# Kernel optimization log

Measured on AMD Instinct MI355X. Metric: run time of the kernel, lower is better.

The kernel has to match this reference:

```python
import jax, jax.numpy as jnp
import numpy as np

IN_DIM = 256
INNER = IN_DIM // 8  # 32


def setup_inputs() -> dict:
    key = jax.random.key(0)
    ks = jax.random.split(key, 9)
    B, C, W, H = 4, IN_DIM, 64, 64
    sc = 0.05
    return {
        "x": jax.random.normal(ks[0], (B, C, W, H), dtype=jnp.float32),
        "Wf": jax.random.normal(ks[1], (INNER, C), dtype=jnp.float32) * sc,
        "bf": jnp.zeros((INNER,), dtype=jnp.float32),
        "Wg": jax.random.normal(ks[2], (INNER, C), dtype=jnp.float32) * sc,
        "bg": jnp.zeros((INNER,), dtype=jnp.float32),
        "Wh": jax.random.normal(ks[3], (INNER, C), dtype=jnp.float32) * sc,
        "bh": jnp.zeros((INNER,), dtype=jnp.float32),
        "Wv": jax.random.normal(ks[4], (C, INNER), dtype=jnp.float32) * sc,
        "bv": jnp.zeros((C,), dtype=jnp.float32),
        "gamma": jnp.ones((1,), dtype=jnp.float32) * 0.5,  # nonzero so attention path matters
    }


def reference(x, Wf, bf, Wg, bg, Wh, bh, Wv, bv, gamma):
    B, C, W, H = x.shape
    N = W * H
    xf = x.reshape(B, C, N)
    # 1x1 convs == per-pixel linear projections
    f = jnp.einsum('kc,bcn->bkn', Wf, xf) + bf[None, :, None]  # [B, C/8, N]
    g = jnp.einsum('kc,bcn->bkn', Wg, xf) + bg[None, :, None]
    h = jnp.einsum('kc,bcn->bkn', Wh, xf) + bh[None, :, None]
    # s[b,n,m] = sum_k f[b,k,n] * g[b,k,m]  (f^T @ g)
    s = jnp.einsum('bkn,bkm->bnm', f, g)                      # [B, N, N]
    attn = jax.nn.softmax(s, axis=-1)                          # softmax over last dim
    attn_map = jnp.transpose(attn, (0, 2, 1))                  # returned map (permuted)
    # o_pre = h_x @ attn_map : o_pre[b,k,m] = sum_n h[b,k,n] * attn[b,m,n]
    o_pre = jnp.einsum('bkn,bmn->bkm', h, attn)                # [B, C/8, N]
    o = jnp.einsum('ck,bkn->bcn', Wv, o_pre) + bv[None, :, None]
    o = o.reshape(B, C, W, H)
    y = gamma.reshape(()) * o + x
    return (y, attn_map)
```

## Files before the change

### kernel.cpp

```cpp
#include <hip/hip_runtime.h>
#include <cstddef>
#include <cstdint>

#define NB     4
#define CDIM   256
#define KD     32
#define NPIX   4096
#define SSHIFT 20.0f

typedef __attribute__((ext_vector_type(8))) short  bfrag;
typedef __attribute__((ext_vector_type(4))) float  facc;

#define MFMA(a,b,c) __builtin_amdgcn_mfma_f32_16x16x32_bf16((a),(b),(c),0,0,0)

__device__ __forceinline__ unsigned short f2bf(float x) {
    union { float f; unsigned u; } v; v.f = x;
    unsigned u = v.u + 0x7fffu + ((v.u >> 16) & 1u);
    return (unsigned short)(u >> 16);
}
__device__ __forceinline__ float bf2f(unsigned short h) {
    union { float f; unsigned u; } v; v.u = ((unsigned)h) << 16;
    return v.f;
}

#define OFF_FA_HI (0)
#define OFF_FA_LO (1u<<20)
#define OFF_GB_HI (2u<<20)
#define OFF_GB_LO (3u<<20)
#define OFF_HB    (4u<<20)
#define OFF_WA_HI (5u<<20)
#define OFF_WA_LO ((5u<<20) + 65536)
#define OFF_OT    ((5u<<20) + 131072)

__global__ __launch_bounds__(256) void wt_kernel(const float* __restrict__ Wf,
                                                 const float* __restrict__ Wg,
                                                 const float* __restrict__ Wh,
                                                 unsigned short* __restrict__ WA_hi,
                                                 unsigned short* __restrict__ WA_lo)
{
    int t = blockIdx.x * 256 + threadIdx.x;
    if (t >= 48 * 64) return;
    int tile = t >> 6, lane = t & 63;
    int rt = tile >> 3, cc = tile & 7;
    int q = lane >> 4, c15 = lane & 15;
    int row = rt * 16 + c15;
    const float* W = (row < 32) ? (Wf + (size_t)row * CDIM)
                   : (row < 64) ? (Wg + (size_t)(row - 32) * CDIM)
                                : (Wh + (size_t)(row - 64) * CDIM);
    int cb = cc * 32 + q * 8;
    bfrag vh, vl;
#pragma unroll
    for (int j = 0; j < 8; ++j) {
        float xv = W[cb + j];
        unsigned short h = f2bf(xv);
        vh[j] = (short)h;
        vl[j] = (short)f2bf(xv - bf2f(h));
    }
    *(bfrag*)(WA_hi + (size_t)t * 8) = vh;
    *(bfrag*)(WA_lo + (size_t)t * 8) = vl;
}

__global__ __launch_bounds__(256) void proj_kernel(const float* __restrict__ x,
                                                   const unsigned short* __restrict__ WA_hi,
                                                   const unsigned short* __restrict__ WA_lo,
                                                   const float* __restrict__ bfv,
                                                   const float* __restrict__ bgv,
                                                   const float* __restrict__ bhv,
                                                   unsigned short* __restrict__ fA_hi,
                                                   unsigned short* __restrict__ fA_lo,
                                                   unsigned short* __restrict__ gB_hi,
                                                   unsigned short* __restrict__ gB_lo,
                                                   unsigned short* __restrict__ hB)
{
    __shared__ float xs[32][65];
    __shared__ float os[96][65];
    __shared__ float bias_s[96];

    const int b  = blockIdx.y;
    const int n0 = blockIdx.x * 64;
    const int tid = threadIdx.x;
    const int w = tid >> 6, lane = tid & 63, q = lane >> 4, c15 = lane & 15;

    if (tid < 96)
        bias_s[tid] = (tid < 32) ? bfv[tid] : (tid < 64 ? bgv[tid - 32] : bhv[tid - 64]);

    facc acc[6];
#pragma unroll
    for (int rt = 0; rt < 6; ++rt) acc[rt] = (facc){0.f, 0.f, 0.f, 0.f};

    const float* xb = x + (size_t)b * CDIM * NPIX + n0;
    const int cr = tid >> 3, nb = (tid & 7) * 8;

    for (int cc = 0; cc < 8; ++cc) {
        const float* src = xb + (size_t)(cc * 32 + cr) * NPIX + nb;
        float4 va = *(const float4*)src;
        float4 vb = *(const float4*)(src + 4);
        __syncthreads();
        *(float4*)&xs[cr][nb]     = va;
        *(float4*)&xs[cr][nb + 4] = vb;
        __syncthreads();

        bfrag xh, xl;
#pragma unroll
        for (int j = 0; j < 8; ++j) {
            float xv = xs[q * 8 + j][w * 16 + c15];
            unsigned short h = f2bf(xv);
            xh[j] = (short)h;
            xl[j] = (short)f2bf(xv - bf2f(h));
        }
#pragma unroll
        for (int rt = 0; rt < 6; ++rt) {
            size_t wo = ((size_t)(rt * 8 + cc) * 64 + lane) * 8;
            bfrag wh = *(const bfrag*)(WA_hi + wo);
            bfrag wl = *(const bfrag*)(WA_lo + wo);
            acc[rt] = MFMA(wh, xh, acc[rt]);
            acc[rt] = MFMA(wh, xl, acc[rt]);
            acc[rt] = MFMA(wl, xh, acc[rt]);
        }
    }

#pragma unroll
    for (int rt = 0; rt < 6; ++rt)
#pragma unroll
        for (int i = 0; i < 4; ++i) {
            int row = rt * 16 + q * 4 + i;
            os[row][w * 16 + c15] = acc[rt][i] + bias_s[row];
        }
    __syncthreads();

    {
        bfrag vh, vl;
#pragma unroll
        for (int j = 0; j < 8; ++j) {
            float v = os[q * 8 + j][w * 16 + c15];
            unsigned short h = f2bf(v);
            vh[j] = (short)h; vl[j] = (short)f2bf(v - bf2f(h));
        }
        size_t o = ((size_t)(b * 256 + (n0 >> 4) + w) * 64 + lane) * 8;
        *(bfrag*)(fA_hi + o) = vh;
        *(bfrag*)(fA_lo + o) = vl;
#pragma unroll
        for (int j = 0; j < 8; ++j) {
            float v = os[32 + q * 8 + j][w * 16 + c15];
            unsigned short h = f2bf(v);
            vh[j] = (short)h; vl[j] = (short)f2bf(v - bf2f(h));
        }
        *(bfrag*)(gB_hi + o) = vh;
        *(bfrag*)(gB_lo + o) = vl;
        int mcl = w >> 1, kt = w & 1;
        bfrag hv;
#pragma unroll
        for (int j = 0; j < 8; ++j) {
            int p = q * 8 + j;
            int mp = (p & 1) * 16 + (p >> 1);
            float v = os[64 + kt * 16 + c15][mcl * 32 + mp];
            hv[j] = (short)f2bf(v);
        }
        size_t oh = ((size_t)((b * 128 + (n0 >> 5) + mcl) * 2 + kt) * 64 + lane) * 8;
        *(bfrag*)(hB + oh) = hv;
    }
}

__global__ __launch_bounds__(256) void attn_kernel(const unsigned short* __restrict__ fA_hi,
                                                   const unsigned short* __restrict__ fA_lo,
                                                   const unsigned short* __restrict__ gB_hi,
                                                   const unsigned short* __restrict__ gB_lo,
                                                   const unsigned short* __restrict__ hB,
                                                   float* __restrict__ am,
                                                   float* __restrict__ oT)
{
    __shared__ unsigned short Pst[4][16 * 40];
    __shared__ float red[4][64][8];
    __shared__ float sums_l[4][16];
    __shared__ float rcp_l[16];
    __shared__ float st2[4][16 * 33];

    const int b  = blockIdx.y;
    const int r0 = blockIdx.x * 16;
    const int tid = threadIdx.x;
    const int w = tid >> 6, lane = tid & 63, q = lane >> 4, c15 = lane & 15;

    const size_t fo = ((size_t)(b * 256 + (r0 >> 4)) * 64 + lane) * 8;
    const bfrag fh = *(const bfrag*)(fA_hi + fo);
    const bfrag fl = *(const bfrag*)(fA_lo + fo);

    facc o0 = (facc){0.f,0.f,0.f,0.f}, o1 = (facc){0.f,0.f,0.f,0.f};
    float sum[4] = {0.f, 0.f, 0.f, 0.f};
    unsigned short* P = &Pst[w][0];

    const int ch0 = w * 32, ch1 = ch0 + 32;

    for (int mc = ch0; mc < ch1; ++mc) {
        size_t go = ((size_t)(b * 256 + 2 * mc) * 64 + lane) * 8;
        bfrag g0h = *(const bfrag*)(gB_hi + go);
        bfrag g1h = *(const bfrag*)(gB_hi + go + 512);
        bfrag g0l = *(const bfrag*)(gB_lo + go);
        bfrag g1l = *(const bfrag*)(gB_lo + go + 512);
        size_t ho = ((size_t)(b * 128 + mc) * 2 * 64 + lane) * 8;
        bfrag h0 = *(const bfrag*)(hB + ho);
        bfrag h1 = *(const bfrag*)(hB + ho + 512);

        facc s0 = (facc){0.f,0.f,0.f,0.f}, s1 = (facc){0.f,0.f,0.f,0.f};
        s0 = MFMA(fh, g0h, s0); s0 = MFMA(fh, g0l, s0); s0 = MFMA(fl, g0h, s0);
        s1 = MFMA(fh, g1h, s1); s1 = MFMA(fh, g1l, s1); s1 = MFMA(fl, g1h, s1);

        float e0[4], e1[4];
#pragma unroll
        for (int i = 0; i < 4; ++i) {
            e0[i] = __expf(s0[i] - SSHIFT);
            e1[i] = __expf(s1[i] - SSHIFT);
            sum[i] += e0[i] + e1[i];
        }
#pragma unroll
        for (int i = 0; i < 4; ++i) {
            unsigned pr = (unsigned)f2bf(e0[i]) | ((unsigned)f2bf(e1[i]) << 16);
            *(unsigned*)&P[(4 * q + i) * 40 + 2 * c15] = pr;
        }
        bfrag pA = *(const bfrag*)&P[c15 * 40 + q * 8];
        o0 = MFMA(pA, h0, o0);
        o1 = MFMA(pA, h1, o1);
    }

#pragma unroll
    for (int m = 1; m < 16; m <<= 1)
#pragma unroll
        for (int i = 0; i < 4; ++i) sum[i] += __shfl_xor(sum[i], m);
    if (c15 == 0) {
#pragma unroll
        for (int i = 0; i < 4; ++i) sums_l[w][4 * q + i] = sum[i];
    }
    *(facc*)&red[w][lane][0] = o0;
    *(facc*)&red[w][lane][4] = o1;
    __syncthreads();
    if (tid < 16)
        rcp_l[tid] = 1.0f / (sums_l[0][tid] + sums_l[1][tid] + sums_l[2][tid] + sums_l[3][tid]);
    __syncthreads();

    float rcpv[4];
#pragma unroll
    for (int i = 0; i < 4; ++i) rcpv[i] = rcp_l[4 * q + i];

    if (w == 0) {
        facc a = (facc){0.f,0.f,0.f,0.f}, bb = (facc){0.f,0.f,0.f,0.f};
#pragma unroll
        for (int ww = 0; ww < 4; ++ww) {
            a  += *(const facc*)&red[ww][lane][0];
            bb += *(const facc*)&red[ww][lane][4];
        }
#pragma unroll
        for (int i = 0; i < 4; ++i) {
            int r = 4 * q + i;
            float rc = rcp_l[r];
            oT[((size_t)(b * NPIX + r0 + r)) * KD + c15]      = a[i] * rc;
            oT[((size_t)(b * NPIX + r0 + r)) * KD + 16 + c15] = bb[i] * rc;
        }
    }

    float* S2 = &st2[w][0];
    const int mr = lane >> 2, ro = (lane & 3) * 4;
    for (int mc = ch0; mc < ch1; ++mc) {
        size_t go = ((size_t)(b * 256 + 2 * mc) * 64 + lane) * 8;
        bfrag g0h = *(const bfrag*)(gB_hi + go);
        bfrag g1h = *(const bfrag*)(gB_hi + go + 512);
        bfrag g0l = *(const bfrag*)(gB_lo + go);
        bfrag g1l = *(const bfrag*)(gB_lo + go + 512);

        facc s0 = (facc){0.f,0.f,0.f,0.f}, s1 = (facc){0.f,0.f,0.f,0.f};
        s0 = MFMA(fh, g0h, s0); s0 = MFMA(fh, g0l, s0); s0 = MFMA(fl, g0h, s0);
        s1 = MFMA(fh, g1h, s1); s1 = MFMA(fh, g1l, s1); s1 = MFMA(fl, g1h, s1);

#pragma unroll
        for (int i = 0; i < 4; ++i) {
            S2[(4 * q + i) * 33 + c15]      = __expf(s0[i] - SSHIFT) * rcpv[i];
            S2[(4 * q + i) * 33 + 16 + c15] = __expf(s1[i] - SSHIFT) * rcpv[i];
        }
        float4 v0, v1;
        v0.x = S2[(ro + 0) * 33 + mr];      v0.y = S2[(ro + 1) * 33 + mr];
        v0.z = S2[(ro + 2) * 33 + mr];      v0.w = S2[(ro + 3) * 33 + mr];
        v1.x = S2[(ro + 0) * 33 + 16 + mr]; v1.y = S2[(ro + 1) * 33 + 16 + mr];
        v1.z = S2[(ro + 2) * 33 + 16 + mr]; v1.w = S2[(ro + 3) * 33 + 16 + mr];
        size_t ao = (size_t)b * NPIX * NPIX + (size_t)(mc * 32 + mr) * NPIX + r0 + ro;
        *(float4*)(am + ao)             = v0;
        *(float4*)(am + ao + 16 * NPIX) = v1;
    }
}

__global__ __launch_bounds__(256) void out_kernel(const float* __restrict__ x,
                                                  const float* __restrict__ oT,
                                                  const float* __restrict__ Wv,
                                                  const float* __restrict__ bv,
                                                  const float* __restrict__ gamma,
                                                  float* __restrict__ y)
{
    __shared__ float wv_s[CDIM * KD];
    const int b  = blockIdx.y;
    const int tid = threadIdx.x;
    const int n = blockIdx.x * 64 + (tid & 63);
    const int cg = tid >> 6;

    for (int i = tid * 4; i < CDIM * KD; i += 1024)
        *(float4*)&wv_s[i] = *(const float4*)&Wv[i];

    float op[KD];
    {
        const float4* src = (const float4*)&oT[((size_t)(b * NPIX + n)) * KD];
#pragma unroll
        for (int qq = 0; qq < 8; ++qq) {
            float4 v = src[qq];
            op[qq * 4 + 0] = v.x; op[qq * 4 + 1] = v.y;
            op[qq * 4 + 2] = v.z; op[qq * 4 + 3] = v.w;
        }
    }
    __syncthreads();
    const float gm = gamma[0];

    for (int c = cg * 64; c < cg * 64 + 64; ++c) {
        float a = 0.f;
#pragma unroll
        for (int k4 = 0; k4 < 8; ++k4) {
            float4 wv4 = *(const float4*)&wv_s[c * KD + k4 * 4];
            a = fmaf(wv4.x, op[k4 * 4 + 0], a);
            a = fmaf(wv4.y, op[k4 * 4 + 1], a);
            a = fmaf(wv4.z, op[k4 * 4 + 2], a);
            a = fmaf(wv4.w, op[k4 * 4 + 3], a);
        }
        size_t idx = ((size_t)(b * CDIM + c)) * NPIX + n;
        y[idx] = fmaf(gm, a + bv[c], x[idx]);
    }
}

extern "C" void kernel_launch(void* const* d_in, const int* in_sizes, int n_in,
                              void* d_out, int out_size, void* d_ws, size_t ws_size,
                              hipStream_t stream)
{
    const float* x     = (const float*)d_in[0];
    const float* Wf    = (const float*)d_in[1];
    const float* bfv   = (const float*)d_in[2];
    const float* Wg    = (const float*)d_in[3];
    const float* bgv   = (const float*)d_in[4];
    const float* Wh    = (const float*)d_in[5];
    const float* bhv   = (const float*)d_in[6];
    const float* Wv    = (const float*)d_in[7];
    const float* bv    = (const float*)d_in[8];
    const float* gamma = (const float*)d_in[9];

    char* ws = (char*)d_ws;
    unsigned short* fA_hi = (unsigned short*)(ws + OFF_FA_HI);
    unsigned short* fA_lo = (unsigned short*)(ws + OFF_FA_LO);
    unsigned short* gB_hi = (unsigned short*)(ws + OFF_GB_HI);
    unsigned short* gB_lo = (unsigned short*)(ws + OFF_GB_LO);
    unsigned short* hB    = (unsigned short*)(ws + OFF_HB);
    unsigned short* WA_hi = (unsigned short*)(ws + OFF_WA_HI);
    unsigned short* WA_lo = (unsigned short*)(ws + OFF_WA_LO);
    float*          oT    = (float*)(ws + OFF_OT);

    float* y  = (float*)d_out;
    float* am = (float*)d_out + (size_t)NB * CDIM * NPIX;

    hipLaunchKernelGGL(wt_kernel, dim3(12), dim3(256), 0, stream, Wf, Wg, Wh, WA_hi, WA_lo);
    hipLaunchKernelGGL(proj_kernel, dim3(NPIX / 64, NB), dim3(256), 0, stream,
                       x, WA_hi, WA_lo, bfv, bgv, bhv, fA_hi, fA_lo, gB_hi, gB_lo, hB);
    hipLaunchKernelGGL(attn_kernel, dim3(NPIX / 16, NB), dim3(256), 0, stream,
                       fA_hi, fA_lo, gB_hi, gB_lo, hB, am, oT);
    hipLaunchKernelGGL(out_kernel, dim3(NPIX / 64, NB), dim3(256), 0, stream,
                       x, oT, Wv, bv, gamma, y);
}
```

Before: 437.8 us.

## Split attention-map write into separate kernel computing transposed scores directly

Moves the attention-map write out of the attention kernel into a new kernel. The new kernel recomputes the scores with g as the A operand and f as the B operand, so each output row is written directly without a shared-memory transpose. The per-row softmax reciprocals are passed between kernels through a workspace buffer. This removes the LDS transpose and its strided stores, at the cost of recomputing the score MFMAs, an extra launch and extra global reads of f fragments and reciprocals.

```diff
diff --git a/kernel.cpp b/kernel.cpp
--- a/kernel.cpp
+++ b/kernel.cpp
@@ -31,6 +31,7 @@
 #define OFF_WA_HI (5u<<20)
 #define OFF_WA_LO ((5u<<20) + 65536)
 #define OFF_OT    ((5u<<20) + 131072)
+#define OFF_RCP   ((5u<<20) + 131072 + (2u<<20))
 
 __global__ __launch_bounds__(256) void wt_kernel(const float* __restrict__ Wf,
                                                  const float* __restrict__ Wg,
@@ -166,14 +167,13 @@
                                                    const unsigned short* __restrict__ gB_hi,
                                                    const unsigned short* __restrict__ gB_lo,
                                                    const unsigned short* __restrict__ hB,
-                                                   float* __restrict__ am,
+                                                   float* __restrict__ rcp_g,
                                                    float* __restrict__ oT)
 {
     __shared__ unsigned short Pst[4][16 * 40];
     __shared__ float red[4][64][8];
     __shared__ float sums_l[4][16];
     __shared__ float rcp_l[16];
-    __shared__ float st2[4][16 * 33];
 
     const int b  = blockIdx.y;
     const int r0 = blockIdx.x * 16;
@@ -232,13 +232,12 @@
     *(facc*)&red[w][lane][0] = o0;
     *(facc*)&red[w][lane][4] = o1;
     __syncthreads();
-    if (tid < 16)
-        rcp_l[tid] = 1.0f / (sums_l[0][tid] + sums_l[1][tid] + sums_l[2][tid] + sums_l[3][tid]);
+    if (tid < 16) {
+        float rv = 1.0f / (sums_l[0][tid] + sums_l[1][tid] + sums_l[2][tid] + sums_l[3][tid]);
+        rcp_l[tid] = rv;
+        rcp_g[(size_t)b * NPIX + r0 + tid] = rv;
+    }
     __syncthreads();
-
-    float rcpv[4];
-#pragma unroll
-    for (int i = 0; i < 4; ++i) rcpv[i] = rcp_l[4 * q + i];
 
     if (w == 0) {
         facc a = (facc){0.f,0.f,0.f,0.f}, bb = (facc){0.f,0.f,0.f,0.f};
@@ -255,33 +254,45 @@
             oT[((size_t)(b * NPIX + r0 + r)) * KD + 16 + c15] = bb[i] * rc;
         }
     }
-
-    float* S2 = &st2[w][0];
-    const int mr = lane >> 2, ro = (lane & 3) * 4;
-    for (int mc = ch0; mc < ch1; ++mc) {
-        size_t go = ((size_t)(b * 256 + 2 * mc) * 64 + lane) * 8;
-        bfrag g0h = *(const bfrag*)(gB_hi + go);
-        bfrag g1h = *(const bfrag*)(gB_hi + go + 512);
-        bfrag g0l = *(const bfrag*)(gB_lo + go);
-        bfrag g1l = *(const bfrag*)(gB_lo + go + 512);
-
-        facc s0 = (facc){0.f,0.f,0.f,0.f}, s1 = (facc){0.f,0.f,0.f,0.f};
-        s0 = MFMA(fh, g0h, s0); s0 = MFMA(fh, g0l, s0); s0 = MFMA(fl, g0h, s0);
-        s1 = MFMA(fh, g1h, s1); s1 = MFMA(fh, g1l, s1); s1 = MFMA(fl, g1h, s1);
-
-#pragma unroll
-        for (int i = 0; i < 4; ++i) {
-            S2[(4 * q + i) * 33 + c15]      = __expf(s0[i] - SSHIFT) * rcpv[i];
-            S2[(4 * q + i) * 33 + 16 + c15] = __expf(s1[i] - SSHIFT) * rcpv[i];
-        }
-        float4 v0, v1;
-        v0.x = S2[(ro + 0) * 33 + mr];      v0.y = S2[(ro + 1) * 33 + mr];
-        v0.z = S2[(ro + 2) * 33 + mr];      v0.w = S2[(ro + 3) * 33 + mr];
-        v1.x = S2[(ro + 0) * 33 + 16 + mr]; v1.y = S2[(ro + 1) * 33 + 16 + mr];
-        v1.z = S2[(ro + 2) * 33 + 16 + mr]; v1.w = S2[(ro + 3) * 33 + 16 + mr];
-        size_t ao = (size_t)b * NPIX * NPIX + (size_t)(mc * 32 + mr) * NPIX + r0 + ro;
-        *(float4*)(am + ao)             = v0;
-        *(float4*)(am + ao + 16 * NPIX) = v1;
+}
+
+__global__ __launch_bounds__(256) void attn2_kernel(const unsigned short* __restrict__ fA_hi,
+                                                    const unsigned short* __restrict__ fA_lo,
+                                                    const unsigned short* __restrict__ gB_hi,
+                                                    const unsigned short* __restrict__ gB_lo,
+                                                    const float* __restrict__ rcp_g,
+                                                    float* __restrict__ am)
+{
+    const int b   = blockIdx.y;
+    const int mt  = blockIdx.x;
+    const int tid = threadIdx.x;
+    const int w = tid >> 6, lane = tid & 63, q = lane >> 4, c15 = lane & 15;
+
+    const size_t ga = ((size_t)(b * 256 + mt) * 64 + lane) * 8;
+    const bfrag a_hi = *(const bfrag*)(gB_hi + ga);
+    const bfrag a_lo = *(const bfrag*)(gB_lo + ga);
+
+    const int m0 = mt * 16 + q * 4;
+    float* amrow = am + (size_t)b * NPIX * NPIX + (size_t)m0 * NPIX;
+    const float* rcp_b = rcp_g + (size_t)b * NPIX;
+
+#pragma unroll 2
+    for (int t = 0; t < 64; ++t) {
+        const int nt = w * 64 + t;
+        const size_t fo = ((size_t)(b * 256 + nt) * 64 + lane) * 8;
+        bfrag b_hi = *(const bfrag*)(fA_hi + fo);
+        bfrag b_lo = *(const bfrag*)(fA_lo + fo);
+
+        facc s = (facc){0.f,0.f,0.f,0.f};
+        s = MFMA(a_hi, b_hi, s);
+        s = MFMA(a_hi, b_lo, s);
+        s = MFMA(a_lo, b_hi, s);
+
+        const int n = nt * 16 + c15;
+        const float rc = rcp_b[n];
+#pragma unroll
+        for (int i = 0; i < 4; ++i)
+            amrow[(size_t)i * NPIX + n] = __expf(s[i] - SSHIFT) * rc;
     }
 }
 
@@ -353,6 +364,7 @@
     unsigned short* WA_hi = (unsigned short*)(ws + OFF_WA_HI);
     unsigned short* WA_lo = (unsigned short*)(ws + OFF_WA_LO);
     float*          oT    = (float*)(ws + OFF_OT);
+    float*          rcp_g = (float*)(ws + OFF_RCP);
 
     float* y  = (float*)d_out;
     float* am = (float*)d_out + (size_t)NB * CDIM * NPIX;
@@ -361,7 +373,9 @@
     hipLaunchKernelGGL(proj_kernel, dim3(NPIX / 64, NB), dim3(256), 0, stream,
                        x, WA_hi, WA_lo, bfv, bgv, bhv, fA_hi, fA_lo, gB_hi, gB_lo, hB);
     hipLaunchKernelGGL(attn_kernel, dim3(NPIX / 16, NB), dim3(256), 0, stream,
-                       fA_hi, fA_lo, gB_hi, gB_lo, hB, am, oT);
+                       fA_hi, fA_lo, gB_hi, gB_lo, hB, rcp_g, oT);
+    hipLaunchKernelGGL(attn2_kernel, dim3(NPIX / 16, NB), dim3(256), 0, stream,
+                       fA_hi, fA_lo, gB_hi, gB_lo, rcp_g, am);
     hipLaunchKernelGGL(out_kernel, dim3(NPIX / 64, NB), dim3(256), 0, stream,
                        x, oT, Wv, bv, gamma, y);
 }
```

Result: faster. 412.3 us (-5.8%).
